# Kernel tuning notes

Measured on AMD Instinct MI355X. Metric: run time of the kernel, lower is better.

## Reference

```python
import jax, jax.numpy as jnp
import numpy as np

B, T, F, H, M = 128, 64, 2048, 1024, 512


def setup_inputs() -> dict:
    key = jax.random.key(0)
    ks = jax.random.split(key, 12)
    def u(k, shape, fan_in):
        s = 1.0 / np.sqrt(fan_in)
        return jax.random.uniform(k, shape, jnp.float32, -s, s)
    return {
        "video_feats": jax.random.normal(ks[0], (B, T, F), jnp.float32),
        # frame_embed: Linear(F -> H)
        "W_embed": u(ks[1], (H, F), F),
        "b_embed": u(ks[2], (H,), F),
        # lstm1_cell: LSTMCell(H, H) with bias (b = b_ih + b_hh, identical math)
        "W_ih1": u(ks[3], (4 * H, H), H),
        "W_hh1": u(ks[4], (4 * H, H), H),
        "b1": u(ks[5], (4 * H,), H),
        # BoundaryDetector(H, H, M): z = sigmoid(vs . (Wsi x + Wsh h + b)), binarized
        "Wsi": u(ks[6], (M, H), H),
        "Wsh": u(ks[7], (M, H), H),
        "b_bd": u(ks[8], (M,), H),
        "vs": u(ks[9], (M,), M),
        # lstm2_cell: LSTMCell(H, H, bias=False)
        "W_ih2": u(ks[10], (4 * H, H), H),
        "W_hh2": u(ks[11], (4 * H, H), H),
    }


def _lstm_cell(x, h, c, W_ih, W_hh, b):
    # PyTorch LSTMCell gate order: i, f, g, o
    gates = x @ W_ih.T + h @ W_hh.T
    if b is not None:
        gates = gates + b
    i, f, g, o = jnp.split(gates, 4, axis=-1)
    c_new = jax.nn.sigmoid(f) * c + jax.nn.sigmoid(i) * jnp.tanh(g)
    h_new = jax.nn.sigmoid(o) * jnp.tanh(c_new)
    return h_new, c_new


def reference(video_feats, W_embed, b_embed, W_ih1, W_hh1, b1,
              Wsi, Wsh, b_bd, vs, W_ih2, W_hh2):
    # frame embedding + ReLU (dropout is identity in eval mode)
    v = jax.nn.relu(jnp.einsum('btf,hf->bth', video_feats, W_embed) + b_embed)
    vt = jnp.transpose(v, (1, 0, 2))  # [T, B, H] for scan over time

    def step(carry, x):
        h1, c1, h2, c2 = carry
        # boundary detector: scalar gate per sample, straight-through binarized
        z = jax.nn.sigmoid((x @ Wsi.T + h1 @ Wsh.T + b_bd) @ vs)  # [B]
        s = (z + jax.lax.stop_gradient(jnp.round(z) - z))[:, None]  # [B,1]
        h1n, c1n = _lstm_cell(x, h1, c1, W_ih1, W_hh1, b1)
        h2n, c2n = _lstm_cell(h1n * s, h2, c2, W_ih2, W_hh2, None)
        h1n = h1n * (1.0 - s)
        c1n = c1n * (1.0 - s)
        return (h1n, c1n, h2n, c2n), None

    z0 = jnp.zeros((B, H), video_feats.dtype)
    (h1, c1, h2, c2), _ = jax.lax.scan(step, (z0, z0, z0, z0), vt)
    return h2
```

## Files before the change

### kernel.cpp

```cpp
#include <hip/hip_runtime.h>
#include <hip/hip_bf16.h>
#include <math.h>


typedef __attribute__((ext_vector_type(8))) short short8;
typedef __attribute__((ext_vector_type(4))) short short4v;
typedef __attribute__((ext_vector_type(4))) float f32x4;
typedef __hip_bfloat16 bf16;

__device__ __forceinline__ float sigm(float x) { return 1.0f / (1.0f + expf(-x)); }
__device__ __forceinline__ short bfbits(float x) {
  bf16 h = __float2bfloat16(x);
  return __builtin_bit_cast(short, h);
}
__device__ __forceinline__ short8 cvt8(const float* __restrict__ p, int mode)
{
  f32x4 a = *(const f32x4*)p;
  f32x4 b = *(const f32x4*)(p + 4);
  short8 r;
#pragma unroll
  for (int j = 0; j < 8; ++j) {
    float x = (j < 4) ? a[j] : b[j - 4];
    if (mode) {
      bf16 h = __float2bfloat16(x);
      x = x - __bfloat162float(h);
    }
    r[j] = bfbits(x);
  }
  return r;
}

__device__ __forceinline__ void gemm_bf16(
    const bf16* __restrict__ A, int lda,
    const bf16* __restrict__ B, int ldb,
    int nChunks, short* ls, f32x4 acc[4][4])
{
  const int tid  = threadIdx.x;
  const int lane = tid & 63;
  const int wave = tid >> 6;
  const int wr = (wave & 1) * 64;
  const int wc = (wave >> 1) * 64;
  const int m  = lane & 15;
  const int kg = lane >> 4;

  int srow[4], sseg[4], ssw[4];
#pragma unroll
  for (int i = 0; i < 4; ++i) {
    int linear = i * 256 + tid;
    srow[i] = linear >> 3;
    sseg[i] = linear & 7;
    ssw[i]  = (sseg[i] ^ (srow[i] & 7)) * 8;
  }

  short8 areg[4], breg[4];
#pragma unroll
  for (int i = 0; i < 4; ++i) {
    areg[i] = *(const short8*)(A + (size_t)srow[i] * lda + sseg[i] * 8);
    breg[i] = *(const short8*)(B + (size_t)srow[i] * ldb + sseg[i] * 8);
  }
#pragma unroll
  for (int i = 0; i < 4; ++i) {
    *(short8*)(ls + srow[i] * 64 + ssw[i])        = areg[i];
    *(short8*)(ls + 8192 + srow[i] * 64 + ssw[i]) = breg[i];
  }
  __syncthreads();

  for (int c = 0; c < nChunks; ++c) {
    if (c + 1 < nChunks) {
#pragma unroll
      for (int i = 0; i < 4; ++i) {
        areg[i] = *(const short8*)(A + (size_t)srow[i] * lda + (c + 1) * 64 + sseg[i] * 8);
        breg[i] = *(const short8*)(B + (size_t)srow[i] * ldb + (c + 1) * 64 + sseg[i] * 8);
      }
    }
    const short* la = ls + (c & 1) * 16384;
    const short* lb = la + 8192;
#pragma unroll
    for (int ks = 0; ks < 2; ++ks) {
      short8 af[4], bfr[4];
#pragma unroll
      for (int f = 0; f < 4; ++f) {
        int ar = wr + f * 16 + m;
        af[f]  = *(const short8*)(la + ar * 64 + (((ks * 4 + kg) ^ (ar & 7)) * 8));
        int br = wc + f * 16 + m;
        bfr[f] = *(const short8*)(lb + br * 64 + (((ks * 4 + kg) ^ (br & 7)) * 8));
      }
#pragma unroll
      for (int fr = 0; fr < 4; ++fr)
#pragma unroll
        for (int fc = 0; fc < 4; ++fc)
          acc[fr][fc] = __builtin_amdgcn_mfma_f32_16x16x32_bf16(af[fr], bfr[fc], acc[fr][fc], 0, 0, 0);
    }
    if (c + 1 < nChunks) {
      short* lw = ls + ((c + 1) & 1) * 16384;
#pragma unroll
      for (int i = 0; i < 4; ++i) {
        *(short8*)(lw + srow[i] * 64 + ssw[i])        = areg[i];
        *(short8*)(lw + 8192 + srow[i] * 64 + ssw[i]) = breg[i];
      }
    }
    __syncthreads();
  }
}

template <typename F>
__device__ __forceinline__ void epilogue(const f32x4 acc[4][4], F&& body)
{
  const int tid = threadIdx.x, lane = tid & 63, wave = tid >> 6;
  const int m = lane & 15, kg = lane >> 4;
  const int wr = (wave & 1) * 64, wc = (wave >> 1) * 64;
#pragma unroll
  for (int fr = 0; fr < 4; ++fr)
#pragma unroll
    for (int fc = 0; fc < 4; ++fc)
#pragma unroll
      for (int r = 0; r < 4; ++r)
        body(wr + fr * 16 + kg * 4 + r, wc + fc * 16 + m, acc[fr][fc][r]);
}

__global__ void k_diag(float* __restrict__ out, float val)
{
  if (threadIdx.x == 0 && blockIdx.x == 0) out[0] = val;
}

__global__ void k_uw(const float* __restrict__ Wsi, const float* __restrict__ Wsh,
                     const float* __restrict__ bbd, const float* __restrict__ vs,
                     double* __restrict__ u, double* __restrict__ wv,
                     double* __restrict__ cbdp)
{
  const int blk = blockIdx.x;
  if (blk < 8) {
    const float* W = (blk < 4) ? Wsi : Wsh;
    double* out = (blk < 4) ? u : wv;
    int h = (blk & 3) * 256 + threadIdx.x;
    double a = 0.0;
    for (int mm = 0; mm < 512; ++mm)
      a += (double)vs[mm] * (double)W[mm * 1024 + h];
    out[h] = a;
  } else if (threadIdx.x < 64) {
    double a = 0.0;
    for (int mm = threadIdx.x; mm < 512; mm += 64)
      a += (double)vs[mm] * (double)bbd[mm];
#pragma unroll
    for (int o = 32; o > 0; o >>= 1) a += __shfl_down(a, o, 64);
    if (threadIdx.x == 0) cbdp[0] = a;
  }
}

__global__ void k_wsplit(const float* __restrict__ w1ih, const float* __restrict__ w1hh,
                         const float* __restrict__ w2ih, const float* __restrict__ w2hh,
                         bf16* __restrict__ o1ih_h, bf16* __restrict__ o1ih_l,
                         bf16* __restrict__ o1hh_h, bf16* __restrict__ o1hh_l,
                         bf16* __restrict__ o2ih_h, bf16* __restrict__ o2hh_h)
{
  const int m = blockIdx.x >> 12;
  const size_t i4 = (size_t)(blockIdx.x & 4095) * 256 + threadIdx.x;
  const float* src = (m == 0) ? w1ih : (m == 1) ? w1hh : (m == 2) ? w2ih : w2hh;
  bf16* dh = (m == 0) ? o1ih_h : (m == 1) ? o1hh_h : (m == 2) ? o2ih_h : o2hh_h;
  bf16* dl = (m == 0) ? o1ih_l : (m == 1) ? o1hh_l : nullptr;
  f32x4 v = *(const f32x4*)(src + i4 * 4);
  short4v hv, lv;
#pragma unroll
  for (int j = 0; j < 4; ++j) {
    float x = v[j];
    bf16 h = __float2bfloat16(x);
    hv[j] = __builtin_bit_cast(short, h);
    lv[j] = bfbits(x - __bfloat162float(h));
  }
  *(short4v*)((short*)dh + i4 * 4) = hv;
  if (dl) *(short4v*)((short*)dl + i4 * 4) = lv;
}

__global__ __launch_bounds__(256, 2) void k_embed(
    const float* __restrict__ video, const float* __restrict__ Wemb,
    const float* __restrict__ bemb, bf16* __restrict__ vhi, bf16* __restrict__ vlo,
    int tbase, int smask)
{
  __shared__ __align__(16) short ls[32768];
  const int t  = tbase + (blockIdx.x >> 3);
  const int ct = blockIdx.x & 7;
  const int tid = threadIdx.x;

  int srow[4], sseg[4], ssw[4];
  const float* arow[4];
  const float* brow[4];
#pragma unroll
  for (int i = 0; i < 4; ++i) {
    int linear = i * 256 + tid;
    srow[i] = linear >> 3;
    sseg[i] = linear & 7;
    ssw[i]  = (sseg[i] ^ (srow[i] & 7)) * 8;
    arow[i] = video + (size_t)(srow[i] * 64 + t) * 2048 + sseg[i] * 8;
    brow[i] = Wemb + (size_t)(ct * 128 + srow[i]) * 2048 + sseg[i] * 8;
  }

  f32x4 acc[4][4] = {};
  const int lane = tid & 63, wave = tid >> 6;
  const int wr = (wave & 1) * 64, wc = (wave >> 1) * 64;
  const int m = lane & 15, kg = lane >> 4;

  short8 areg[4], breg[4];
#pragma unroll
  for (int i = 0; i < 4; ++i) {
    areg[i] = cvt8(arow[i], 0);
    breg[i] = cvt8(brow[i], 0);
  }
#pragma unroll
  for (int i = 0; i < 4; ++i) {
    *(short8*)(ls + srow[i] * 64 + ssw[i])        = areg[i];
    *(short8*)(ls + 8192 + srow[i] * 64 + ssw[i]) = breg[i];
  }
  __syncthreads();

  for (int q = 0; q < 96; ++q) {
    if (q + 1 < 96) {
      int pn = (q + 1) >> 5, cn = (q + 1) & 31;
      int am = (pn == 1), bm = (pn == 2);
#pragma unroll
      for (int i = 0; i < 4; ++i) {
        areg[i] = cvt8(arow[i] + cn * 64, am);
        breg[i] = cvt8(brow[i] + cn * 64, bm);
      }
    }
    const short* la = ls + (q & 1) * 16384;
    const short* lb = la + 8192;
#pragma unroll
    for (int ks = 0; ks < 2; ++ks) {
      short8 af[4], bfr[4];
#pragma unroll
      for (int f = 0; f < 4; ++f) {
        int ar = wr + f * 16 + m;
        af[f]  = *(const short8*)(la + ar * 64 + (((ks * 4 + kg) ^ (ar & 7)) * 8));
        int br = wc + f * 16 + m;
        bfr[f] = *(const short8*)(lb + br * 64 + (((ks * 4 + kg) ^ (br & 7)) * 8));
      }
#pragma unroll
      for (int fr = 0; fr < 4; ++fr)
#pragma unroll
        for (int fc = 0; fc < 4; ++fc)
          acc[fr][fc] = __builtin_amdgcn_mfma_f32_16x16x32_bf16(af[fr], bfr[fc], acc[fr][fc], 0, 0, 0);
    }
    if (q + 1 < 96) {
      short* lw = ls + ((q + 1) & 1) * 16384;
#pragma unroll
      for (int i = 0; i < 4; ++i) {
        *(short8*)(lw + srow[i] * 64 + ssw[i])        = areg[i];
        *(short8*)(lw + 8192 + srow[i] * 64 + ssw[i]) = breg[i];
      }
    }
    __syncthreads();
  }

  const int trow = (t & smask) * 128;
  epilogue(acc, [&](int lrow, int lcol, float aval) {
    int gcol = ct * 128 + lcol;
    float x = fmaxf(aval + bemb[gcol], 0.0f);
    bf16 hi = __float2bfloat16(x);
    size_t o = (size_t)(trow + lrow) * 1024 + gcol;
    vhi[o] = hi;
    vlo[o] = __float2bfloat16(x - __bfloat162float(hi));
  });
}

__global__ void k_zx(const bf16* __restrict__ vhi, const bf16* __restrict__ vlo,
                     const double* __restrict__ u, const double* __restrict__ cbdp,
                     float* __restrict__ zx, int base)
{
  const int wave = blockIdx.x * 4 + (threadIdx.x >> 6);
  const int lane = threadIdx.x & 63;
  for (int it = 0; it < 16; ++it) {
    int rr = wave * 16 + it;
    double a = 0.0;
#pragma unroll
    for (int q = 0; q < 16; ++q) {
      int h = lane + q * 64;
      size_t o = (size_t)rr * 1024 + h;
      a += (double)(__bfloat162float(vhi[o]) + __bfloat162float(vlo[o])) * u[h];
    }
#pragma unroll
    for (int o = 32; o > 0; o >>= 1) a += __shfl_down(a, o, 64);
    if (lane == 0) zx[base + rr] = (float)(a + cbdp[0]);
  }
}

__global__ __launch_bounds__(256, 2) void k_step(
    const bf16* __restrict__ vhi, const bf16* __restrict__ vlo,
    const bf16* __restrict__ h1r1h, const bf16* __restrict__ h1r1l,
    const bf16* __restrict__ h1r2h, const bf16* __restrict__ h1r2l,
    const bf16* __restrict__ h2h, const bf16* __restrict__ h2l,
    const bf16* __restrict__ w1ih_h, const bf16* __restrict__ w1ih_l,
    const bf16* __restrict__ w1hh_h, const bf16* __restrict__ w1hh_l,
    const bf16* __restrict__ w2ih_h, const bf16* __restrict__ w2hh_h,
    float* __restrict__ R, int k, int smask)
{
  __shared__ __align__(16) short ls[32768];
  const bf16* vh = vhi + (size_t)(k & smask) * 131072;
  const bf16* vl = vlo + (size_t)(k & smask) * 131072;

  for (int u = blockIdx.x; u < 320; u += 256) {
    const int p  = u >> 5;
    const int ct = u & 31;
    if (k == 64 && p < 6) continue;
    if (k == 0 && p >= 3) continue;

    const bf16 *A, *B;
    switch (p) {
      case 0: A = vh;    B = w1ih_h; break;
      case 1: A = vl;    B = w1ih_h; break;
      case 2: A = vh;    B = w1ih_l; break;
      case 3: A = h1r1h; B = w1hh_h; break;
      case 4: A = h1r1l; B = w1hh_h; break;
      case 5: A = h1r1h; B = w1hh_l; break;
      case 6: A = h1r2h; B = w2ih_h; break;
      case 7: A = h1r2l; B = w2ih_h; break;
      case 8: A = h2h;   B = w2hh_h; break;
      default: A = h2l;  B = w2hh_h; break;
    }
    f32x4 acc[4][4] = {};
    gemm_bf16(A, 1024, B + (size_t)ct * 131072, 1024, 16, ls, acc);
    float* Rout = R + (size_t)p * 524288;
    epilogue(acc, [&](int lrow, int lcol, float aval) {
      Rout[(size_t)lrow * 4096 + ct * 128 + lcol] = aval;
    });
  }
}

__global__ void k_elem(const float* __restrict__ R, const float* __restrict__ zx,
                       float* __restrict__ craw,
                       bf16* __restrict__ h1r1h, bf16* __restrict__ h1r1l,
                       bf16* __restrict__ h1r2h, bf16* __restrict__ h1r2l,
                       float* __restrict__ c2, bf16* __restrict__ h2h, bf16* __restrict__ h2l,
                       float* __restrict__ rdm, const double* __restrict__ wv,
                       const float* __restrict__ b1, float* __restrict__ dout, int k)
{
  __shared__ double red[4];
  const int tid = threadIdx.x;
  const int b   = blockIdx.x;
  const size_t broff = (size_t)b * 4096;
  const float* P0 = R + broff;
  const float* P1 = P0 + 524288;
  const float* P2 = P0 + 2 * 524288;
  const float* P3 = P0 + 3 * 524288;
  const float* P4 = P0 + 4 * 524288;
  const float* P5 = P0 + 5 * 524288;
  const float* P6 = P0 + 6 * 524288;
  const float* P7 = P0 + 7 * 524288;
  const float* P8 = P0 + 8 * 524288;
  const float* P9 = P0 + 9 * 524288;

  if (k < 64) {
    float zpre = zx[k * 128 + b];
    if (k > 0) zpre += rdm[(k - 1) * 128 + b];
    float s  = (sigm(zpre) > 0.5f) ? 1.0f : 0.0f;
    float om = 1.0f - s;

    double rd = 0.0;
#pragma unroll
    for (int ji = 0; ji < 4; ++ji) {
      int j = tid + ji * 256;
      float gi = P0[j]        + P1[j]        + P2[j]        + b1[j];
      float gf = P0[1024 + j] + P1[1024 + j] + P2[1024 + j] + b1[1024 + j];
      float gg = P0[2048 + j] + P1[2048 + j] + P2[2048 + j] + b1[2048 + j];
      float go = P0[3072 + j] + P1[3072 + j] + P2[3072 + j] + b1[3072 + j];
      if (k > 0) {
        gi += P3[j]        + P4[j]        + P5[j];
        gf += P3[1024 + j] + P4[1024 + j] + P5[1024 + j];
        gg += P3[2048 + j] + P4[2048 + j] + P5[2048 + j];
        go += P3[3072 + j] + P4[3072 + j] + P5[3072 + j];
      }
      float cn = sigm(gf) * craw[b * 1024 + j] + sigm(gi) * tanhf(gg);
      float hn = sigm(go) * tanhf(cn);
      craw[b * 1024 + j] = om * cn;
      float v1 = om * hn;
      bf16 h1 = __float2bfloat16(v1);
      h1r1h[b * 1024 + j] = h1;
      h1r1l[b * 1024 + j] = __float2bfloat16(v1 - __bfloat162float(h1));
      float v2 = s * hn;
      bf16 h2v = __float2bfloat16(v2);
      h1r2h[b * 1024 + j] = h2v;
      h1r2l[b * 1024 + j] = __float2bfloat16(v2 - __bfloat162float(h2v));
      rd += (double)hn * wv[j];
    }
#pragma unroll
    for (int o = 32; o > 0; o >>= 1) rd += __shfl_down(rd, o, 64);
    if ((tid & 63) == 0) red[tid >> 6] = rd;
    __syncthreads();
    if (tid == 0)
      rdm[k * 128 + b] = om * (float)(red[0] + red[1] + red[2] + red[3]);
  }

  if (k >= 1) {
#pragma unroll
    for (int ji = 0; ji < 4; ++ji) {
      int j = tid + ji * 256;
      float gi = P6[j]        + P7[j]        + P8[j]        + P9[j];
      float gf = P6[1024 + j] + P7[1024 + j] + P8[1024 + j] + P9[1024 + j];
      float gg = P6[2048 + j] + P7[2048 + j] + P8[2048 + j] + P9[2048 + j];
      float go = P6[3072 + j] + P7[3072 + j] + P8[3072 + j] + P9[3072 + j];
      float cn = sigm(gf) * c2[b * 1024 + j] + sigm(gi) * tanhf(gg);
      float hn = sigm(go) * tanhf(cn);
      c2[b * 1024 + j] = cn;
      bf16 hh = __float2bfloat16(hn);
      h2h[b * 1024 + j] = hh;
      h2l[b * 1024 + j] = __float2bfloat16(hn - __bfloat162float(hh));
      if (k == 64) dout[b * 1024 + j] = hn;
    }
  }
}

extern "C" void kernel_launch(void* const* d_in, const int* in_sizes, int n_in,
                              void* d_out, int out_size, void* d_ws, size_t ws_size,
                              hipStream_t stream) {
  const float* video = (const float*)d_in[0];
  const float* Wemb  = (const float*)d_in[1];
  const float* bemb  = (const float*)d_in[2];
  const float* Wih1  = (const float*)d_in[3];
  const float* Whh1  = (const float*)d_in[4];
  const float* b1    = (const float*)d_in[5];
  const float* Wsi   = (const float*)d_in[6];
  const float* Wsh   = (const float*)d_in[7];
  const float* bbd   = (const float*)d_in[8];
  const float* vs    = (const float*)d_in[9];
  const float* Wih2  = (const float*)d_in[10];
  const float* Whh2  = (const float*)d_in[11];
  float* dout = (float*)d_out;

  static const int exp_sizes[12] = {
    128 * 64 * 2048, 1024 * 2048, 1024, 4096 * 1024, 4096 * 1024, 4096,
    512 * 1024, 512 * 1024, 512, 512, 4096 * 1024, 4096 * 1024 };
  int bad = -1;
  if (n_in != 12) bad = 99;
  else if (out_size != 131072) bad = 98;
  else
    for (int i = 0; i < 12; ++i)
      if (in_sizes[i] != exp_sizes[i]) { bad = i; break; }
  if (bad >= 0) {
    k_diag<<<1, 64, 0, stream>>>(dout, 10000.0f + (float)bad);
    return;
  }

  char* ws = (char*)d_ws;
  size_t off = 0;
  auto alloc = [&](size_t bytes) {
    char* p = ws + off;
    off += (bytes + 255) & ~(size_t)255;
    return p;
  };
  bf16*  h1r1h = (bf16*)alloc(262144);
  bf16*  h1r1l = (bf16*)alloc(262144);
  bf16*  h1r2h = (bf16*)alloc(262144);
  bf16*  h1r2l = (bf16*)alloc(262144);
  bf16*  h2h   = (bf16*)alloc(262144);
  bf16*  h2l   = (bf16*)alloc(262144);
  float* c2    = (float*)alloc(524288);
  float* craw  = (float*)alloc(524288);
  const size_t zeroBytes = off;
  double* u    = (double*)alloc(8192);
  double* wvv  = (double*)alloc(8192);
  double* cbdp = (double*)alloc(256);
  float* rdm   = (float*)alloc(64 * 128 * 4);
  float* zx    = (float*)alloc(8192 * 4);
  bf16* w1ih_h = (bf16*)alloc(8388608);
  bf16* w1ih_l = (bf16*)alloc(8388608);
  bf16* w1hh_h = (bf16*)alloc(8388608);
  bf16* w1hh_l = (bf16*)alloc(8388608);
  bf16* w2ih_h = (bf16*)alloc(8388608);
  bf16* w2hh_h = (bf16*)alloc(8388608);
  float* R     = (float*)alloc(10 * 524288 * 4);
  const size_t fixedBytes = off;

  const size_t need_small = fixedBytes + 2 * ((size_t)8 * 131072 * 2 + 256);
  const size_t need_full  = fixedBytes + 2 * ((size_t)64 * 131072 * 2 + 256);
  if (ws_size < need_small) {
    k_diag<<<1, 64, 0, stream>>>(dout, 100.0f + (float)(ws_size >> 20));
    return;
  }
  const bool fullv = (ws_size >= need_full);
  const int slots = fullv ? 64 : 8;
  const int smask = slots - 1;
  bf16* vhi = (bf16*)alloc((size_t)slots * 131072 * 2);
  bf16* vlo = (bf16*)alloc((size_t)slots * 131072 * 2);

  (void)hipMemsetAsync(d_ws, 0, zeroBytes, stream);
  k_uw<<<9, 256, 0, stream>>>(Wsi, Wsh, bbd, vs, u, wvv, cbdp);
  k_wsplit<<<16384, 256, 0, stream>>>(Wih1, Whh1, Wih2, Whh2,
                                      w1ih_h, w1ih_l, w1hh_h, w1hh_l, w2ih_h, w2hh_h);
  if (fullv) {
    k_embed<<<512, 256, 0, stream>>>(video, Wemb, bemb, vhi, vlo, 0, smask);
    k_zx<<<128, 256, 0, stream>>>(vhi, vlo, u, cbdp, zx, 0);
  }

  for (int k = 0; k <= 64; ++k) {
    if (!fullv && k < 64 && (k & 7) == 0) {
      k_embed<<<64, 256, 0, stream>>>(video, Wemb, bemb, vhi, vlo, k, smask);
      k_zx<<<16, 256, 0, stream>>>(vhi, vlo, u, cbdp, zx, k * 128);
    }
    k_step<<<256, 256, 0, stream>>>(vhi, vlo, h1r1h, h1r1l, h1r2h, h1r2l, h2h, h2l,
                                    w1ih_h, w1ih_l, w1hh_h, w1hh_l, w2ih_h, w2hh_h,
                                    R, k, smask);
    k_elem<<<128, 256, 0, stream>>>(R, zx, craw, h1r1h, h1r1l, h1r2h, h1r2l,
                                    c2, h2h, h2l, rdm, wvv, b1, dout, k);
  }
}
```

Before: 3.268 ms.

## Fuse split-precision GEMM passes in embed and pair step GEMMs per block

The embed kernel now builds the hi and lo bf16 parts of both operands in one pass over K. It keeps all four parts in LDS and issues the three product MFMAs (hh, lh, hl) per chunk, instead of streaming 96 chunks with separate passes. Each step-kernel block now accumulates two GEMM partials into one accumulator, which halves the R buffer, the grid (160 blocks) and the partial sums k_elem has to read. The slot count for the embedding buffer adapts to workspace size. The costs are an extra barrier in embed, lost double buffering, and serialized work per step block.

```diff
diff --git a/kernel.cpp b/kernel.cpp
--- a/kernel.cpp
+++ b/kernel.cpp
@@ -13,21 +13,18 @@
   bf16 h = __float2bfloat16(x);
   return __builtin_bit_cast(short, h);
 }
-__device__ __forceinline__ short8 cvt8(const float* __restrict__ p, int mode)
+__device__ __forceinline__ void cvt8hl(const float* __restrict__ p,
+                                       short8& hi, short8& lo)
 {
   f32x4 a = *(const f32x4*)p;
   f32x4 b = *(const f32x4*)(p + 4);
-  short8 r;
 #pragma unroll
   for (int j = 0; j < 8; ++j) {
     float x = (j < 4) ? a[j] : b[j - 4];
-    if (mode) {
-      bf16 h = __float2bfloat16(x);
-      x = x - __bfloat162float(h);
-    }
-    r[j] = bfbits(x);
-  }
-  return r;
+    bf16 h = __float2bfloat16(x);
+    hi[j] = __builtin_bit_cast(short, h);
+    lo[j] = bfbits(x - __bfloat162float(h));
+  }
 }
 
 __device__ __forceinline__ void gemm_bf16(
@@ -199,56 +196,75 @@
   const int wr = (wave & 1) * 64, wc = (wave >> 1) * 64;
   const int m = lane & 15, kg = lane >> 4;
 
-  short8 areg[4], breg[4];
+  short8 ah[4], al[4], bh[4], bl[4];
 #pragma unroll
   for (int i = 0; i < 4; ++i) {
-    areg[i] = cvt8(arow[i], 0);
-    breg[i] = cvt8(brow[i], 0);
+    cvt8hl(arow[i], ah[i], al[i]);
+    cvt8hl(brow[i], bh[i], bl[i]);
   }
 #pragma unroll
   for (int i = 0; i < 4; ++i) {
-    *(short8*)(ls + srow[i] * 64 + ssw[i])        = areg[i];
-    *(short8*)(ls + 8192 + srow[i] * 64 + ssw[i]) = breg[i];
+    *(short8*)(ls +         srow[i] * 64 + ssw[i]) = ah[i];
+    *(short8*)(ls +  8192 + srow[i] * 64 + ssw[i]) = al[i];
+    *(short8*)(ls + 16384 + srow[i] * 64 + ssw[i]) = bh[i];
+    *(short8*)(ls + 24576 + srow[i] * 64 + ssw[i]) = bl[i];
   }
   __syncthreads();
 
-  for (int q = 0; q < 96; ++q) {
-    if (q + 1 < 96) {
-      int pn = (q + 1) >> 5, cn = (q + 1) & 31;
-      int am = (pn == 1), bm = (pn == 2);
+  for (int c = 0; c < 32; ++c) {
+    if (c + 1 < 32) {
 #pragma unroll
       for (int i = 0; i < 4; ++i) {
-        areg[i] = cvt8(arow[i] + cn * 64, am);
-        breg[i] = cvt8(brow[i] + cn * 64, bm);
-      }
-    }
-    const short* la = ls + (q & 1) * 16384;
-    const short* lb = la + 8192;
+        cvt8hl(arow[i] + (c + 1) * 64, ah[i], al[i]);
+        cvt8hl(brow[i] + (c + 1) * 64, bh[i], bl[i]);
+      }
+    }
 #pragma unroll
     for (int ks = 0; ks < 2; ++ks) {
-      short8 af[4], bfr[4];
+      short8 afh[4], afl[4], bfh[4], bfl[4];
+      int asw[4], bsw[4];
 #pragma unroll
       for (int f = 0; f < 4; ++f) {
         int ar = wr + f * 16 + m;
-        af[f]  = *(const short8*)(la + ar * 64 + (((ks * 4 + kg) ^ (ar & 7)) * 8));
+        asw[f] = ar * 64 + (((ks * 4 + kg) ^ (ar & 7)) * 8);
         int br = wc + f * 16 + m;
-        bfr[f] = *(const short8*)(lb + br * 64 + (((ks * 4 + kg) ^ (br & 7)) * 8));
+        bsw[f] = br * 64 + (((ks * 4 + kg) ^ (br & 7)) * 8);
+        afh[f] = *(const short8*)(ls +         asw[f]);
+        bfh[f] = *(const short8*)(ls + 16384 + bsw[f]);
       }
 #pragma unroll
       for (int fr = 0; fr < 4; ++fr)
 #pragma unroll
         for (int fc = 0; fc < 4; ++fc)
-          acc[fr][fc] = __builtin_amdgcn_mfma_f32_16x16x32_bf16(af[fr], bfr[fc], acc[fr][fc], 0, 0, 0);
-    }
-    if (q + 1 < 96) {
-      short* lw = ls + ((q + 1) & 1) * 16384;
+          acc[fr][fc] = __builtin_amdgcn_mfma_f32_16x16x32_bf16(afh[fr], bfh[fc], acc[fr][fc], 0, 0, 0);
+#pragma unroll
+      for (int f = 0; f < 4; ++f)
+        afl[f] = *(const short8*)(ls + 8192 + asw[f]);
+#pragma unroll
+      for (int fr = 0; fr < 4; ++fr)
+#pragma unroll
+        for (int fc = 0; fc < 4; ++fc)
+          acc[fr][fc] = __builtin_amdgcn_mfma_f32_16x16x32_bf16(afl[fr], bfh[fc], acc[fr][fc], 0, 0, 0);
+#pragma unroll
+      for (int f = 0; f < 4; ++f)
+        bfl[f] = *(const short8*)(ls + 24576 + bsw[f]);
+#pragma unroll
+      for (int fr = 0; fr < 4; ++fr)
+#pragma unroll
+        for (int fc = 0; fc < 4; ++fc)
+          acc[fr][fc] = __builtin_amdgcn_mfma_f32_16x16x32_bf16(afh[fr], bfl[fc], acc[fr][fc], 0, 0, 0);
+    }
+    if (c + 1 < 32) {
+      __syncthreads();
 #pragma unroll
       for (int i = 0; i < 4; ++i) {
-        *(short8*)(lw + srow[i] * 64 + ssw[i])        = areg[i];
-        *(short8*)(lw + 8192 + srow[i] * 64 + ssw[i]) = breg[i];
-      }
-    }
-    __syncthreads();
+        *(short8*)(ls +         srow[i] * 64 + ssw[i]) = ah[i];
+        *(short8*)(ls +  8192 + srow[i] * 64 + ssw[i]) = al[i];
+        *(short8*)(ls + 16384 + srow[i] * 64 + ssw[i]) = bh[i];
+        *(short8*)(ls + 24576 + srow[i] * 64 + ssw[i]) = bl[i];
+      }
+      __syncthreads();
+    }
   }
 
   const int trow = (t & smask) * 128;
@@ -297,32 +313,29 @@
   const bf16* vh = vhi + (size_t)(k & smask) * 131072;
   const bf16* vl = vlo + (size_t)(k & smask) * 131072;
 
-  for (int u = blockIdx.x; u < 320; u += 256) {
-    const int p  = u >> 5;
-    const int ct = u & 31;
-    if (k == 64 && p < 6) continue;
-    if (k == 0 && p >= 3) continue;
-
-    const bf16 *A, *B;
-    switch (p) {
-      case 0: A = vh;    B = w1ih_h; break;
-      case 1: A = vl;    B = w1ih_h; break;
-      case 2: A = vh;    B = w1ih_l; break;
-      case 3: A = h1r1h; B = w1hh_h; break;
-      case 4: A = h1r1l; B = w1hh_h; break;
-      case 5: A = h1r1h; B = w1hh_l; break;
-      case 6: A = h1r2h; B = w2ih_h; break;
-      case 7: A = h1r2l; B = w2ih_h; break;
-      case 8: A = h2h;   B = w2hh_h; break;
-      default: A = h2l;  B = w2hh_h; break;
-    }
-    f32x4 acc[4][4] = {};
-    gemm_bf16(A, 1024, B + (size_t)ct * 131072, 1024, 16, ls, acc);
-    float* Rout = R + (size_t)p * 524288;
-    epilogue(acc, [&](int lrow, int lcol, float aval) {
-      Rout[(size_t)lrow * 4096 + ct * 128 + lcol] = aval;
-    });
-  }
+  const int pr = blockIdx.x >> 5;
+  const int ct = blockIdx.x & 31;
+  if (k == 0 && pr >= 2) return;
+  if (k == 64 && pr < 3) return;
+
+  const bf16 *A0, *B0, *A1, *B1;
+  switch (pr) {
+    case 0:  A0 = vh;    B0 = w1ih_h; A1 = vl;    B1 = w1ih_h; break;
+    case 1:  A0 = vh;    B0 = w1ih_l; A1 = h1r1h; B1 = w1hh_h; break;
+    case 2:  A0 = h1r1l; B0 = w1hh_h; A1 = h1r1h; B1 = w1hh_l; break;
+    case 3:  A0 = h1r2h; B0 = w2ih_h; A1 = h1r2l; B1 = w2ih_h; break;
+    default: A0 = h2h;   B0 = w2hh_h; A1 = h2l;   B1 = w2hh_h; break;
+  }
+
+  f32x4 acc[4][4] = {};
+  gemm_bf16(A0, 1024, B0 + (size_t)ct * 131072, 1024, 16, ls, acc);
+  if (!(k == 0 && pr == 1))
+    gemm_bf16(A1, 1024, B1 + (size_t)ct * 131072, 1024, 16, ls, acc);
+
+  float* Rout = R + (size_t)pr * 524288;
+  epilogue(acc, [&](int lrow, int lcol, float aval) {
+    Rout[(size_t)lrow * 4096 + ct * 128 + lcol] = aval;
+  });
 }
 
 __global__ void k_elem(const float* __restrict__ R, const float* __restrict__ zx,
@@ -342,11 +355,6 @@
   const float* P2 = P0 + 2 * 524288;
   const float* P3 = P0 + 3 * 524288;
   const float* P4 = P0 + 4 * 524288;
-  const float* P5 = P0 + 5 * 524288;
-  const float* P6 = P0 + 6 * 524288;
-  const float* P7 = P0 + 7 * 524288;
-  const float* P8 = P0 + 8 * 524288;
-  const float* P9 = P0 + 9 * 524288;
 
   if (k < 64) {
     float zpre = zx[k * 128 + b];
@@ -358,15 +366,15 @@
 #pragma unroll
     for (int ji = 0; ji < 4; ++ji) {
       int j = tid + ji * 256;
-      float gi = P0[j]        + P1[j]        + P2[j]        + b1[j];
-      float gf = P0[1024 + j] + P1[1024 + j] + P2[1024 + j] + b1[1024 + j];
-      float gg = P0[2048 + j] + P1[2048 + j] + P2[2048 + j] + b1[2048 + j];
-      float go = P0[3072 + j] + P1[3072 + j] + P2[3072 + j] + b1[3072 + j];
+      float gi = P0[j]        + P1[j]        + b1[j];
+      float gf = P0[1024 + j] + P1[1024 + j] + b1[1024 + j];
+      float gg = P0[2048 + j] + P1[2048 + j] + b1[2048 + j];
+      float go = P0[3072 + j] + P1[3072 + j] + b1[3072 + j];
       if (k > 0) {
-        gi += P3[j]        + P4[j]        + P5[j];
-        gf += P3[1024 + j] + P4[1024 + j] + P5[1024 + j];
-        gg += P3[2048 + j] + P4[2048 + j] + P5[2048 + j];
-        go += P3[3072 + j] + P4[3072 + j] + P5[3072 + j];
+        gi += P2[j];
+        gf += P2[1024 + j];
+        gg += P2[2048 + j];
+        go += P2[3072 + j];
       }
       float cn = sigm(gf) * craw[b * 1024 + j] + sigm(gi) * tanhf(gg);
       float hn = sigm(go) * tanhf(cn);
@@ -393,10 +401,10 @@
 #pragma unroll
     for (int ji = 0; ji < 4; ++ji) {
       int j = tid + ji * 256;
-      float gi = P6[j]        + P7[j]        + P8[j]        + P9[j];
-      float gf = P6[1024 + j] + P7[1024 + j] + P8[1024 + j] + P9[1024 + j];
-      float gg = P6[2048 + j] + P7[2048 + j] + P8[2048 + j] + P9[2048 + j];
-      float go = P6[3072 + j] + P7[3072 + j] + P8[3072 + j] + P9[3072 + j];
+      float gi = P3[j]        + P4[j];
+      float gf = P3[1024 + j] + P4[1024 + j];
+      float gg = P3[2048 + j] + P4[2048 + j];
+      float go = P3[3072 + j] + P4[3072 + j];
       float cn = sigm(gf) * c2[b * 1024 + j] + sigm(gi) * tanhf(gg);
       float hn = sigm(go) * tanhf(cn);
       c2[b * 1024 + j] = cn;
@@ -466,17 +474,17 @@
   bf16* w1hh_l = (bf16*)alloc(8388608);
   bf16* w2ih_h = (bf16*)alloc(8388608);
   bf16* w2hh_h = (bf16*)alloc(8388608);
-  float* R     = (float*)alloc(10 * 524288 * 4);
+  float* R     = (float*)alloc(5 * 524288 * 4);
   const size_t fixedBytes = off;
 
-  const size_t need_small = fixedBytes + 2 * ((size_t)8 * 131072 * 2 + 256);
-  const size_t need_full  = fixedBytes + 2 * ((size_t)64 * 131072 * 2 + 256);
-  if (ws_size < need_small) {
+  const size_t perSlot = (size_t)131072 * 2 * 2;
+  int slots = 64;
+  while (slots > 8 && fixedBytes + (size_t)slots * perSlot + 512 > ws_size)
+    slots >>= 1;
+  if (fixedBytes + (size_t)8 * perSlot + 512 > ws_size) {
     k_diag<<<1, 64, 0, stream>>>(dout, 100.0f + (float)(ws_size >> 20));
     return;
   }
-  const bool fullv = (ws_size >= need_full);
-  const int slots = fullv ? 64 : 8;
   const int smask = slots - 1;
   bf16* vhi = (bf16*)alloc((size_t)slots * 131072 * 2);
   bf16* vlo = (bf16*)alloc((size_t)slots * 131072 * 2);
@@ -485,17 +493,17 @@
   k_uw<<<9, 256, 0, stream>>>(Wsi, Wsh, bbd, vs, u, wvv, cbdp);
   k_wsplit<<<16384, 256, 0, stream>>>(Wih1, Whh1, Wih2, Whh2,
                                       w1ih_h, w1ih_l, w1hh_h, w1hh_l, w2ih_h, w2hh_h);
-  if (fullv) {
+  if (slots == 64) {
     k_embed<<<512, 256, 0, stream>>>(video, Wemb, bemb, vhi, vlo, 0, smask);
     k_zx<<<128, 256, 0, stream>>>(vhi, vlo, u, cbdp, zx, 0);
   }
 
   for (int k = 0; k <= 64; ++k) {
-    if (!fullv && k < 64 && (k & 7) == 0) {
-      k_embed<<<64, 256, 0, stream>>>(video, Wemb, bemb, vhi, vlo, k, smask);
-      k_zx<<<16, 256, 0, stream>>>(vhi, vlo, u, cbdp, zx, k * 128);
-    }
-    k_step<<<256, 256, 0, stream>>>(vhi, vlo, h1r1h, h1r1l, h1r2h, h1r2l, h2h, h2l,
+    if (slots < 64 && k < 64 && (k & smask) == 0) {
+      k_embed<<<slots * 8, 256, 0, stream>>>(video, Wemb, bemb, vhi, vlo, k, smask);
+      k_zx<<<slots * 2, 256, 0, stream>>>(vhi, vlo, u, cbdp, zx, k * 128);
+    }
+    k_step<<<160, 256, 0, stream>>>(vhi, vlo, h1r1h, h1r1l, h1r2h, h1r2l, h2h, h2l,
                                     w1ih_h, w1ih_l, w1hh_h, w1hh_l, w2ih_h, w2hh_h,
                                     R, k, smask);
     k_elem<<<128, 256, 0, stream>>>(R, zx, craw, h1r1h, h1r1l, h1r2h, h1r2l,
```

After: 3.087 ms. -5.5%, faster.
